# Kernel optimization log

Hardware: AMD Instinct MI355X
Metric: run time of the kernel (lower is better)

Reference implementation:

```python
import jax, jax.numpy as jnp
import numpy as np

EPS = 1e-6
LN3 = 1.0986122886681098  # ternary_softmax uses base-3 exponentials: 3**x / sum(3**x)
ROPE_BASE = 10000.0


def exact_rmsnorm(x, g):
    # ExactRMSNorm: x / sqrt(mean(x^2) + eps) * g
    ms = jnp.mean(jnp.square(x), axis=-1, keepdims=True)
    return x * jax.lax.rsqrt(ms + EPS) * g


def ternary_rope(t):
    # Rotary embedding whose cos/sin tables are quantized to {-1, 0, +1}
    # (round() of cos/sin in [-1,1] yields exactly the ternary set).
    S, D = t.shape[-2], t.shape[-1]
    half = D // 2
    inv_freq = 1.0 / (ROPE_BASE ** (jnp.arange(half, dtype=jnp.float32) / half))
    ang = jnp.arange(S, dtype=jnp.float32)[:, None] * inv_freq[None, :]  # [S, half]
    cos = jnp.round(jnp.cos(ang))
    sin = jnp.round(jnp.sin(ang))
    cos = jnp.concatenate([cos, cos], axis=-1)  # [S, D]
    sin = jnp.concatenate([sin, sin], axis=-1)
    rot = jnp.concatenate([-t[..., half:], t[..., :half]], axis=-1)
    return t * cos + rot * sin


def ternary_softmax(x, axis=-1):
    # softmax in base 3: 3**x / sum(3**x) == softmax(x * ln 3)
    return jax.nn.softmax(x * LN3, axis=axis)


def setup_inputs() -> dict:
    key = jax.random.key(0)
    ks = jax.random.split(key, 6)
    B, S, D = 4, 4096, 1024
    x = jax.random.normal(ks[0], (B, S, D), dtype=jnp.float32)
    g_norm = jnp.ones((D,), dtype=jnp.float32)
    w_qkv = jax.random.normal(ks[1], (D, 3 * D), dtype=jnp.float32) * 0.02
    b_qkv = jnp.zeros((3 * D,), dtype=jnp.float32)
    w_proj = jax.random.normal(ks[2], (D, D), dtype=jnp.float32) * 0.02
    b_proj = jnp.zeros((D,), dtype=jnp.float32)
    return {"x": x, "g_norm": g_norm, "w_qkv": w_qkv, "b_qkv": b_qkv,
            "w_proj": w_proj, "b_proj": b_proj}


def reference(x, g_norm, w_qkv, b_qkv, w_proj, b_proj):
    D = x.shape[-1]
    scale = 1.0 / jnp.sqrt(jnp.float32(D))
    residual = x
    h = exact_rmsnorm(x, g_norm)
    qkv = h @ w_qkv + b_qkv  # [B, S, 3D]
    q, k, v = jnp.split(qkv, 3, axis=-1)
    q = ternary_rope(q)
    k = ternary_rope(k)
    scores = jnp.einsum("bsd,btd->bst", q, k) * scale  # [B, S, S]
    attn = ternary_softmax(scores, axis=-1)
    o = jnp.einsum("bst,btd->bsd", attn, v)
    return o @ w_proj + b_proj + residual
```

## Files before the change

kernel.cpp:

```cpp
#include <hip/hip_runtime.h>
#include <hip/hip_fp8.h>
#include <stdint.h>

#define DEVI __device__ __forceinline__

typedef unsigned short u16;
typedef uint8_t u8;
typedef __attribute__((ext_vector_type(8))) __bf16 bf16x8;
typedef __attribute__((ext_vector_type(4))) float f32x4;
typedef __attribute__((ext_vector_type(4))) int i32x4;
typedef __attribute__((ext_vector_type(8))) int i32x8;

DEVI float b2f(u16 u) { union { unsigned int i; float f; } v; v.i = ((unsigned int)u) << 16; return v.f; }
DEVI u16 f2b(float f) {
  union { float f; unsigned int i; } v; v.f = f;
  unsigned int r = v.i + 0x7fffu + ((v.i >> 16) & 1u);
  return (u16)(r >> 16);
}
DEVI u8 f2f8(float f) { __hip_fp8_e4m3 t(f); return t.__x; }

DEVI void gld_lds16(const void* g, void* l) {
  __builtin_amdgcn_global_load_lds((const __attribute__((address_space(1))) unsigned int*)g,
                                   (__attribute__((address_space(3))) unsigned int*)l, 16, 0, 0);
}

DEVI i32x8 ld32(const u8* p0, const u8* p1) {
  i32x4 lo = *(const i32x4*)p0;
  i32x4 hi = *(const i32x4*)p1;
  return __builtin_shufflevector(lo, hi, 0, 1, 2, 3, 4, 5, 6, 7);
}


__global__ __launch_bounds__(256) void k_rmsnorm(const float* __restrict__ x,
                                                 const float* __restrict__ g,
                                                 u8* __restrict__ h) {
  const int row = blockIdx.x;
  const int t = threadIdx.x;
  const float4 v = ((const float4*)(x + (size_t)row * 1024))[t];
  float ss = v.x * v.x + v.y * v.y + v.z * v.z + v.w * v.w;
  for (int off = 32; off > 0; off >>= 1) ss += __shfl_down(ss, off);
  __shared__ float red[4];
  if ((t & 63) == 0) red[t >> 6] = ss;
  __syncthreads();
  const float tot = red[0] + red[1] + red[2] + red[3];
  const float sc = rsqrtf(tot * (1.0f / 1024.0f) + 1e-6f);
  const float4 gv = ((const float4*)g)[t];
  uchar4 o;
  o.x = f2f8(v.x * sc * gv.x); o.y = f2f8(v.y * sc * gv.y);
  o.z = f2f8(v.z * sc * gv.z); o.w = f2f8(v.w * sc * gv.w);
  *(uchar4*)(h + (size_t)row * 1024 + t * 4) = o;
}

__global__ __launch_bounds__(256) void k_transpose_cast(const float* __restrict__ src,
                                                        int rows, int cols,
                                                        u16* __restrict__ dst) {
  __shared__ float tile[32][33];
  const int c0 = blockIdx.x * 32, r0 = blockIdx.y * 32;
  const int tx = threadIdx.x, ty = threadIdx.y;
  for (int i = 0; i < 32; i += 8)
    tile[ty + i][tx] = src[(size_t)(r0 + ty + i) * cols + c0 + tx];
  __syncthreads();
  for (int i = 0; i < 32; i += 8)
    dst[(size_t)(c0 + ty + i) * rows + r0 + tx] = f2b(tile[tx][ty + i]);
}

__global__ __launch_bounds__(256) void k_transpose_cast_f8(const float* __restrict__ src,
                                                           int rows, int cols,
                                                           u8* __restrict__ dst) {
  __shared__ float tile[32][33];
  const int c0 = blockIdx.x * 32, r0 = blockIdx.y * 32;
  const int tx = threadIdx.x, ty = threadIdx.y;
  for (int i = 0; i < 32; i += 8)
    tile[ty + i][tx] = src[(size_t)(r0 + ty + i) * cols + c0 + tx];
  __syncthreads();
  for (int i = 0; i < 32; i += 8)
    dst[(size_t)(c0 + ty + i) * rows + r0 + tx] = f2f8(tile[tx][ty + i] * 32.0f);
}

__global__ __launch_bounds__(256) void k_rope_cast(const u16* __restrict__ q16, const u16* __restrict__ k16,
                                                   u8* __restrict__ q8, u8* __restrict__ k8) {
  const int row = blockIdx.x;
  const int pos = row & 4095;
  const int t = threadIdx.x;
  const int j0 = t * 2;
  float c[2], s[2];
#pragma unroll
  for (int u = 0; u < 2; u++) {
    const float e = (float)(j0 + u) * (1.0f / 512.0f);
    const float invf = exp2f(-13.287712379549449f * e);
    const float ang = (float)pos * invf;
    c[u] = rintf(cosf(ang));
    s[u] = rintf(sinf(ang));
  }
  const u16* qr = q16 + (size_t)row * 1024;
  const u16* kr = k16 + (size_t)row * 1024;
  u8* qo = q8 + (size_t)row * 1024;
  u8* ko = k8 + (size_t)row * 1024;
  const ushort2 qa = *(const ushort2*)(qr + j0), qb = *(const ushort2*)(qr + j0 + 512);
  const ushort2 ka = *(const ushort2*)(kr + j0), kb = *(const ushort2*)(kr + j0 + 512);
  uchar2 o;
  o.x = f2f8(b2f(qa.x) * c[0] - b2f(qb.x) * s[0]);
  o.y = f2f8(b2f(qa.y) * c[1] - b2f(qb.y) * s[1]);
  *(uchar2*)(qo + j0) = o;
  o.x = f2f8(b2f(qb.x) * c[0] + b2f(qa.x) * s[0]);
  o.y = f2f8(b2f(qb.y) * c[1] + b2f(qa.y) * s[1]);
  *(uchar2*)(qo + j0 + 512) = o;
  o.x = f2f8(b2f(ka.x) * c[0] - b2f(kb.x) * s[0]);
  o.y = f2f8(b2f(ka.y) * c[1] - b2f(kb.y) * s[1]);
  *(uchar2*)(ko + j0) = o;
  o.x = f2f8(b2f(kb.x) * c[0] + b2f(ka.x) * s[0]);
  o.y = f2f8(b2f(kb.y) * c[1] + b2f(ka.y) * s[1]);
  *(uchar2*)(ko + j0 + 512) = o;
}

DEVI void gemm_tile(const u16* __restrict__ A, int lda,
                    const u16* __restrict__ B, int ldb,
                    int K, int m0, int n0,
                    u16* As, u16* Bs, f32x4 acc[4][4]) {
  const int t = threadIdx.x;
  const int sr = t >> 2;
  const int sc = (t & 3) * 8;
  const u16* Ag0 = A + (size_t)(m0 + sr) * lda + sc;
  const u16* Ag1 = A + (size_t)(m0 + 64 + sr) * lda + sc;
  const u16* Bg0 = B + (size_t)(n0 + sr) * ldb + sc;
  const u16* Bg1 = B + (size_t)(n0 + 64 + sr) * ldb + sc;
  u16* Asw = As + t * 8;
  u16* Bsw = Bs + t * 8;

  const int lane = t & 63, qd = lane >> 4, l16 = lane & 15;
  const int wave = t >> 6;
  const int wm = (wave >> 1) * 64, wn = (wave & 1) * 64;
  const int aoff = (wm + l16) * 32 + qd * 8;
  const int boff = (wn + l16) * 32 + qd * 8;

  auto stage = [&](int sel, int k0) {
    u16* Ad = Asw + sel * 4096;
    u16* Bd = Bsw + sel * 4096;
    gld_lds16(Ag0 + k0, Ad);
    gld_lds16(Ag1 + k0, Ad + 2048);
    gld_lds16(Bg0 + k0, Bd);
    gld_lds16(Bg1 + k0, Bd + 2048);
  };

  stage(0, 0);
  int cur = 0;
  for (int k0 = 0; k0 < K; k0 += 32) {
    if (k0 + 32 < K) {
      stage(cur ^ 1, k0 + 32);
      asm volatile("s_waitcnt vmcnt(4)" ::: "memory");
    } else {
      asm volatile("s_waitcnt vmcnt(0)" ::: "memory");
    }
    __builtin_amdgcn_s_barrier();
    const u16* Ard = As + cur * 4096 + aoff;
    const u16* Brd = Bs + cur * 4096 + boff;
    bf16x8 af[4], bfv[4];
#pragma unroll
    for (int i = 0; i < 4; i++) af[i] = *(const bf16x8*)(Ard + i * 16 * 32);
#pragma unroll
    for (int j = 0; j < 4; j++) bfv[j] = *(const bf16x8*)(Brd + j * 16 * 32);
    __builtin_amdgcn_s_setprio(1);
#pragma unroll
    for (int i = 0; i < 4; i++)
#pragma unroll
      for (int j = 0; j < 4; j++)
        acc[i][j] = __builtin_amdgcn_mfma_f32_16x16x32_bf16(af[i], bfv[j], acc[i][j], 0, 0, 0);
    __builtin_amdgcn_s_setprio(0);
    __builtin_amdgcn_s_barrier();
    cur ^= 1;
  }
}

DEVI void gemm_tile_mx(const u8* __restrict__ A, int lda,
                       const u8* __restrict__ B, int ldb,
                       int K, int m0, int n0,
                       u8* As, u8* Bs, f32x4 acc[4][4], int sB) {
  const int t = threadIdx.x;
  const int sr = t >> 3;
  const int sc = ((t & 7) ^ (sr & 7)) << 4;
  const u8* Agb = A + (size_t)(m0 + sr) * lda + sc;
  const u8* Bgb = B + (size_t)(n0 + sr) * ldb + sc;
  u8* Asw = As + t * 16;
  u8* Bsw = Bs + t * 16;

  const int lane = t & 63, qd = lane >> 4, l16 = lane & 15;
  const int wave = t >> 6;
  const int wm = (wave >> 1) * 64, wn = (wave & 1) * 64;
  const int key = l16 & 7;
  const int c0 = ((qd << 1) ^ key) << 4;
  const int aoff = (wm + l16) * 128 + c0;
  const int boff = (wn + l16) * 128 + c0;

  auto stage = [&](int sel, int k0) {
    u8* Ad = Asw + sel * 16384;
    u8* Bd = Bsw + sel * 16384;
#pragma unroll
    for (int l = 0; l < 4; l++) {
      gld_lds16(Agb + k0 + (size_t)l * 32 * lda, Ad + l * 4096);
      gld_lds16(Bgb + k0 + (size_t)l * 32 * ldb, Bd + l * 4096);
    }
  };

  stage(0, 0);
  int cur = 0;
  for (int k0 = 0; k0 < K; k0 += 128) {
    if (k0 + 128 < K) {
      stage(cur ^ 1, k0 + 128);
      asm volatile("s_waitcnt vmcnt(8)" ::: "memory");
    } else {
      asm volatile("s_waitcnt vmcnt(0)" ::: "memory");
    }
    __builtin_amdgcn_s_barrier();
    const u8* Ab = As + cur * 16384;
    const u8* Bb = Bs + cur * 16384;
    i32x8 a[4], b[4];
#pragma unroll
    for (int i = 0; i < 4; i++)
      a[i] = ld32(Ab + aoff + i * 2048, Ab + (aoff ^ 16) + i * 2048);
#pragma unroll
    for (int j = 0; j < 4; j++)
      b[j] = ld32(Bb + boff + j * 2048, Bb + (boff ^ 16) + j * 2048);
    __builtin_amdgcn_s_setprio(1);
#pragma unroll
    for (int i = 0; i < 4; i++)
#pragma unroll
      for (int j = 0; j < 4; j++)
        acc[i][j] = __builtin_amdgcn_mfma_scale_f32_16x16x128_f8f6f4(
            a[i], b[j], acc[i][j], 0 , 0 ,
            0, 0x7f7f7f7f, 0, sB);
    __builtin_amdgcn_s_setprio(0);
    __builtin_amdgcn_s_barrier();
    cur ^= 1;
  }
}

#define ACC_INIT()                                               \
  f32x4 acc[4][4];                                               \
  _Pragma("unroll") for (int i = 0; i < 4; i++)                  \
      _Pragma("unroll") for (int j = 0; j < 4; j++)              \
          acc[i][j] = f32x4{0.f, 0.f, 0.f, 0.f};

#define GEMM_EPI_IDX()                                           \
  const int t = threadIdx.x, lane = t & 63, qd = lane >> 4,      \
            l16 = lane & 15, wave = t >> 6;                      \
  const int wm = (wave >> 1) * 64, wn = (wave & 1) * 64;         \
  (void)t;


__global__ __launch_bounds__(256) void k_gemm_qkv(const u8* __restrict__ A, const u8* __restrict__ Bt,
                                                  const float* __restrict__ bias,
                                                  u16* __restrict__ q16, u16* __restrict__ k16,
                                                  u8* __restrict__ vt) {
  __shared__ alignas(16) u8 As[32768], Bs[32768];
  ACC_INIT();
  const int bid = blockIdx.y * 24 + blockIdx.x;
  const int xcd = bid & 7, idx = bid >> 3;
  const int m0 = (xcd * 16 + idx / 24) * 128;
  const int n0 = (idx % 24) * 128;
  gemm_tile_mx(A, 1024, Bt, 1024, 1024, m0, n0, As, Bs, acc, 0x7a7a7a7a);
  GEMM_EPI_IDX();
  const int sec = n0 >> 10;
  const int nb0 = n0 & 1023;
  if (sec < 2) {
    u16* dst = (sec == 0) ? q16 : k16;
#pragma unroll
    for (int i = 0; i < 4; i++) {
      const int mb = m0 + wm + i * 16 + qd * 4;
#pragma unroll
      for (int j = 0; j < 4; j++) {
        const int col = n0 + wn + j * 16 + l16;
        const float bv = bias[col];
        const int dcol = nb0 + wn + j * 16 + l16;
#pragma unroll
        for (int r = 0; r < 4; r++)
          dst[(size_t)(mb + r) * 1024 + dcol] = f2b(acc[i][j][r] + bv);
      }
    }
  } else {
    u8* T = As;
    const int STR = 144;
#pragma unroll
    for (int i = 0; i < 4; i++) {
      const int mloc = wm + i * 16 + qd * 4;
#pragma unroll
      for (int j = 0; j < 4; j++) {
        const int dloc = wn + j * 16 + l16;
        const float bv = bias[n0 + wn + j * 16 + l16];
#pragma unroll
        for (int r = 0; r < 4; r++)
          T[dloc * STR + mloc + r] = f2f8(acc[i][j][r] + bv);
      }
    }
    __syncthreads();
    const int b = m0 >> 12;
    const int s0 = m0 & 4095;
    const int row = t >> 1, half = (t & 1) * 64;
    u8* dst = vt + ((size_t)(b * 1024 + nb0 + row)) * 4096 + s0 + half;
#pragma unroll
    for (int c = 0; c < 4; c++)
      *(i32x4*)(dst + c * 16) = *(const i32x4*)(T + row * STR + half + c * 16);
  }
}

__global__ __launch_bounds__(256) void k_gemm_scores(const u8* __restrict__ q, const u8* __restrict__ kk,
                                                     u8* __restrict__ P, float* __restrict__ ls) {
  __shared__ alignas(16) u8 As[32768], Bs[32768];
  ACC_INIT();
  const int b = blockIdx.z;
  const u8* A = q + (size_t)b * 4096 * 1024;
  const u8* Bt = kk + (size_t)b * 4096 * 1024;
  const int bid = blockIdx.y * 32 + blockIdx.x;
  const int xcd = bid & 7, idx = bid >> 3;
  const int m0 = ((xcd >> 2) * 16 + (idx & 15)) * 128;
  const int n0 = ((xcd & 3) * 8 + (idx >> 4)) * 128;
  gemm_tile_mx(A, 1024, Bt, 1024, 1024, m0, n0, As, Bs, acc, 0x7f7f7f7f);
  GEMM_EPI_IDX();
  const float C3 = 0.04953007814753613f;
  const size_t Pb = (size_t)b * 4096 * 4096;
  f32x4 rowp[4];
#pragma unroll
  for (int i = 0; i < 4; i++) rowp[i] = f32x4{0.f, 0.f, 0.f, 0.f};
#pragma unroll
  for (int i = 0; i < 4; i++) {
    const int mb = m0 + wm + i * 16 + qd * 4;
#pragma unroll
    for (int j = 0; j < 4; j++) {
      const int col = n0 + wn + j * 16 + l16;
#pragma unroll
      for (int r = 0; r < 4; r++) {
        const float pv = __builtin_amdgcn_exp2f(acc[i][j][r] * C3);
        P[Pb + (size_t)(mb + r) * 4096 + col] = f2f8(pv);
        rowp[i][r] += pv;
      }
    }
  }
#pragma unroll
  for (int m = 1; m < 16; m <<= 1)
#pragma unroll
    for (int i = 0; i < 4; i++) {
      rowp[i].x += __shfl_xor(rowp[i].x, m);
      rowp[i].y += __shfl_xor(rowp[i].y, m);
      rowp[i].z += __shfl_xor(rowp[i].z, m);
      rowp[i].w += __shfl_xor(rowp[i].w, m);
    }
  if (l16 == 0) {
#pragma unroll
    for (int i = 0; i < 4; i++) {
      const int mb = m0 + wm + i * 16 + qd * 4;
#pragma unroll
      for (int r = 0; r < 4; r++)
        atomicAdd(ls + (size_t)b * 4096 + mb + r, rowp[i][r]);
    }
  }
}

__global__ __launch_bounds__(256) void k_gemm_pv(const u8* __restrict__ P, const u8* __restrict__ vt,
                                                 const float* __restrict__ ls, u16* __restrict__ o) {
  __shared__ alignas(16) u8 As[32768], Bs[32768];
  ACC_INIT();
  const int b = blockIdx.z;
  const u8* A = P + (size_t)b * 4096 * 4096;
  const u8* Bt = vt + (size_t)b * 1024 * 4096;
  const int bid = blockIdx.y * 8 + blockIdx.x;
  const int xcd = bid & 7, idx = bid >> 3;
  const int m0 = ((xcd >> 1) * 8 + (idx & 7)) * 128;
  const int n0 = ((xcd & 1) * 4 + (idx >> 3)) * 128;
  gemm_tile_mx(A, 4096, Bt, 4096, 4096, m0, n0, As, Bs, acc, 0x7f7f7f7f);
  GEMM_EPI_IDX();
#pragma unroll
  for (int i = 0; i < 4; i++) {
    const int mb = m0 + wm + i * 16 + qd * 4;
    f32x4 inv;
#pragma unroll
    for (int r = 0; r < 4; r++) inv[r] = 1.0f / ls[(size_t)b * 4096 + mb + r];
#pragma unroll
    for (int j = 0; j < 4; j++) {
      const int col = n0 + wn + j * 16 + l16;
#pragma unroll
      for (int r = 0; r < 4; r++)
        o[(size_t)(b * 4096 + mb + r) * 1024 + col] = f2b(acc[i][j][r] * inv[r]);
    }
  }
}

__global__ __launch_bounds__(256) void k_gemm_proj(const u16* __restrict__ A, const u16* __restrict__ Bt,
                                                   const float* __restrict__ bias, const float* __restrict__ x,
                                                   float* __restrict__ out) {
  __shared__ alignas(16) u16 As[8192], Bs[8192];
  ACC_INIT();
  const int bid = blockIdx.y * 8 + blockIdx.x;
  const int xcd = bid & 7, idx = bid >> 3;
  const int m0 = (xcd * 16 + idx / 8) * 128;
  const int n0 = (idx % 8) * 128;
  gemm_tile(A, 1024, Bt, 1024, 1024, m0, n0, As, Bs, acc);
  GEMM_EPI_IDX();
#pragma unroll
  for (int i = 0; i < 4; i++) {
    const int mb = m0 + wm + i * 16 + qd * 4;
#pragma unroll
    for (int j = 0; j < 4; j++) {
      const int col = n0 + wn + j * 16 + l16;
      const float bv = bias[col];
#pragma unroll
      for (int r = 0; r < 4; r++) {
        const size_t idxo = (size_t)(mb + r) * 1024 + col;
        out[idxo] = acc[i][j][r] + bv + x[idxo];
      }
    }
  }
}

extern "C" void kernel_launch(void* const* d_in, const int* in_sizes, int n_in,
                              void* d_out, int out_size, void* d_ws, size_t ws_size,
                              hipStream_t stream) {
  const float* x     = (const float*)d_in[0];
  const float* g     = (const float*)d_in[1];
  const float* wqkv  = (const float*)d_in[2];
  const float* bqkv  = (const float*)d_in[3];
  const float* wproj = (const float*)d_in[4];
  const float* bproj = (const float*)d_in[5];
  float* out = (float*)d_out;

  char* wsp = (char*)d_ws;
  size_t off = 0;
  auto take = [&](size_t bytes) -> void* {
    off = (off + 255) & ~(size_t)255;
    void* r = wsp + off;
    off += bytes;
    return r;
  };
  char* hreg = (char*)take(16384ull * 1024 * 2);
  u8*  h8   = (u8*)hreg;
  u16* o16  = (u16*)hreg;
  u8*  wqT8 = (u8*)take(3072ull * 1024);
  u16* wpT  = (u16*)take(1024ull * 1024 * 2);
  u8*  q8   = (u8*)take(16384ull * 1024);
  u8*  k8   = (u8*)take(16384ull * 1024);
  u8*  vt   = (u8*)take(4ull * 1024 * 4096);
  float* ls = (float*)take(16384ull * 4);
  char* scratch = (char*)take(3ull * 16384 * 1024 * 2);
  u16* q16 = (u16*)scratch;
  u16* k16 = (u16*)(scratch + 16384ull * 1024 * 2);
  u8*  P   = (u8*)scratch;

  k_transpose_cast_f8<<<dim3(3072 / 32, 1024 / 32), dim3(32, 8), 0, stream>>>(wqkv, 1024, 3072, wqT8);
  k_transpose_cast<<<dim3(1024 / 32, 1024 / 32), dim3(32, 8), 0, stream>>>(wproj, 1024, 1024, wpT);
  k_rmsnorm<<<16384, 256, 0, stream>>>(x, g, h8);
  k_gemm_qkv<<<dim3(24, 128), 256, 0, stream>>>(h8, wqT8, bqkv, q16, k16, vt);
  k_rope_cast<<<16384, 256, 0, stream>>>(q16, k16, q8, k8);
  hipMemsetAsync(ls, 0, 16384 * 4, stream);
  k_gemm_scores<<<dim3(32, 32, 4), 256, 0, stream>>>(q8, k8, P, ls);
  k_gemm_pv<<<dim3(8, 32, 4), 256, 0, stream>>>(P, vt, ls, o16);
  k_gemm_proj<<<dim3(8, 128), 256, 0, stream>>>(o16, wpT, bproj, x, out);
}
```

Before: 450.6 us.

## Fuse ternary RoPE into QKV GEMM epilogue via permuted weight columns

Permutes the Q/K columns of the transposed fp8 QKV weight so each rotary pair lands in adjacent lanes. The GEMM epilogue then applies the rotation with a lane shuffle and a precomputed ternary cos/sin table, writing fp8 Q/K directly. This removes the separate rope_cast kernel and the bf16 Q/K round trip through global memory. In exchange it adds a small table-building kernel and per-element table loads and byte-sized scattered stores in the epilogue.

Result: no change. 455.6 us (+1.1%).

```diff
diff --git a/kernel.cpp b/kernel.cpp
--- a/kernel.cpp
+++ b/kernel.cpp
@@ -64,6 +64,13 @@
     dst[(size_t)(c0 + ty + i) * rows + r0 + tx] = f2b(tile[tx][ty + i]);
 }
 
+DEVI int rope_perm(int c) {
+  if (c >= 2048) return c;
+  const int sec = c >> 10, cc = c & 1023;
+  const int slot = (cc < 512) ? (cc << 1) : (((cc - 512) << 1) | 1);
+  return (sec << 10) | slot;
+}
+
 __global__ __launch_bounds__(256) void k_transpose_cast_f8(const float* __restrict__ src,
                                                            int rows, int cols,
                                                            u8* __restrict__ dst) {
@@ -74,43 +81,23 @@
     tile[ty + i][tx] = src[(size_t)(r0 + ty + i) * cols + c0 + tx];
   __syncthreads();
   for (int i = 0; i < 32; i += 8)
-    dst[(size_t)(c0 + ty + i) * rows + r0 + tx] = f2f8(tile[tx][ty + i] * 32.0f);
-}
-
-__global__ __launch_bounds__(256) void k_rope_cast(const u16* __restrict__ q16, const u16* __restrict__ k16,
-                                                   u8* __restrict__ q8, u8* __restrict__ k8) {
-  const int row = blockIdx.x;
-  const int pos = row & 4095;
+    dst[(size_t)rope_perm(c0 + ty + i) * rows + r0 + tx] = f2f8(tile[tx][ty + i] * 32.0f);
+}
+
+__global__ __launch_bounds__(256) void k_rope_table(char2* __restrict__ tab) {
+  const int pos = blockIdx.x;
   const int t = threadIdx.x;
-  const int j0 = t * 2;
-  float c[2], s[2];
 #pragma unroll
   for (int u = 0; u < 2; u++) {
-    const float e = (float)(j0 + u) * (1.0f / 512.0f);
+    const int m = t * 2 + u;
+    const float e = (float)m * (1.0f / 512.0f);
     const float invf = exp2f(-13.287712379549449f * e);
     const float ang = (float)pos * invf;
-    c[u] = rintf(cosf(ang));
-    s[u] = rintf(sinf(ang));
-  }
-  const u16* qr = q16 + (size_t)row * 1024;
-  const u16* kr = k16 + (size_t)row * 1024;
-  u8* qo = q8 + (size_t)row * 1024;
-  u8* ko = k8 + (size_t)row * 1024;
-  const ushort2 qa = *(const ushort2*)(qr + j0), qb = *(const ushort2*)(qr + j0 + 512);
-  const ushort2 ka = *(const ushort2*)(kr + j0), kb = *(const ushort2*)(kr + j0 + 512);
-  uchar2 o;
-  o.x = f2f8(b2f(qa.x) * c[0] - b2f(qb.x) * s[0]);
-  o.y = f2f8(b2f(qa.y) * c[1] - b2f(qb.y) * s[1]);
-  *(uchar2*)(qo + j0) = o;
-  o.x = f2f8(b2f(qb.x) * c[0] + b2f(qa.x) * s[0]);
-  o.y = f2f8(b2f(qb.y) * c[1] + b2f(qa.y) * s[1]);
-  *(uchar2*)(qo + j0 + 512) = o;
-  o.x = f2f8(b2f(ka.x) * c[0] - b2f(kb.x) * s[0]);
-  o.y = f2f8(b2f(ka.y) * c[1] - b2f(kb.y) * s[1]);
-  *(uchar2*)(ko + j0) = o;
-  o.x = f2f8(b2f(kb.x) * c[0] + b2f(ka.x) * s[0]);
-  o.y = f2f8(b2f(kb.y) * c[1] + b2f(ka.y) * s[1]);
-  *(uchar2*)(ko + j0 + 512) = o;
+    char2 cs;
+    cs.x = (char)rintf(cosf(ang));
+    cs.y = (char)rintf(sinf(ang));
+    tab[(size_t)pos * 512 + m] = cs;
+  }
 }
 
 DEVI void gemm_tile(const u16* __restrict__ A, int lda,
@@ -249,7 +236,8 @@
 
 __global__ __launch_bounds__(256) void k_gemm_qkv(const u8* __restrict__ A, const u8* __restrict__ Bt,
                                                   const float* __restrict__ bias,
-                                                  u16* __restrict__ q16, u16* __restrict__ k16,
+                                                  const char2* __restrict__ tab,
+                                                  u8* __restrict__ q8, u8* __restrict__ k8,
                                                   u8* __restrict__ vt) {
   __shared__ alignas(16) u8 As[32768], Bs[32768];
   ACC_INIT();
@@ -262,18 +250,28 @@
   const int sec = n0 >> 10;
   const int nb0 = n0 & 1023;
   if (sec < 2) {
-    u16* dst = (sec == 0) ? q16 : k16;
+    u8* dst = (sec == 0) ? q8 : k8;
 #pragma unroll
     for (int i = 0; i < 4; i++) {
       const int mb = m0 + wm + i * 16 + qd * 4;
 #pragma unroll
       for (int j = 0; j < 4; j++) {
-        const int col = n0 + wn + j * 16 + l16;
-        const float bv = bias[col];
-        const int dcol = nb0 + wn + j * 16 + l16;
-#pragma unroll
-        for (int r = 0; r < 4; r++)
-          dst[(size_t)(mb + r) * 1024 + dcol] = f2b(acc[i][j][r] + bv);
+        const int pc = nb0 + wn + j * 16 + l16;
+        const int m = pc >> 1;
+        const int par = pc & 1;
+        const int ocol = m + (par << 9);
+        const float bv = bias[(sec << 10) + ocol];
+#pragma unroll
+        for (int r = 0; r < 4; r++) {
+          const int row = mb + r;
+          const int pos = row & 4095;
+          const float v = acc[i][j][r] + bv;
+          const float p = __shfl_xor(v, 1);
+          const char2 cs = tab[(size_t)pos * 512 + m];
+          const float c = (float)cs.x, s = (float)cs.y;
+          const float out = par ? (v * c + p * s) : (v * c - p * s);
+          dst[(size_t)row * 1024 + ocol] = f2f8(out);
+        }
       }
     }
   } else {
@@ -295,10 +293,10 @@
     const int b = m0 >> 12;
     const int s0 = m0 & 4095;
     const int row = t >> 1, half = (t & 1) * 64;
-    u8* dst = vt + ((size_t)(b * 1024 + nb0 + row)) * 4096 + s0 + half;
+    u8* dstv = vt + ((size_t)(b * 1024 + (n0 & 1023) + row)) * 4096 + s0 + half;
 #pragma unroll
     for (int c = 0; c < 4; c++)
-      *(i32x4*)(dst + c * 16) = *(const i32x4*)(T + row * STR + half + c * 16);
+      *(i32x4*)(dstv + c * 16) = *(const i32x4*)(T + row * STR + half + c * 16);
   }
 }
 
@@ -438,16 +436,14 @@
   u8*  k8   = (u8*)take(16384ull * 1024);
   u8*  vt   = (u8*)take(4ull * 1024 * 4096);
   float* ls = (float*)take(16384ull * 4);
-  char* scratch = (char*)take(3ull * 16384 * 1024 * 2);
-  u16* q16 = (u16*)scratch;
-  u16* k16 = (u16*)(scratch + 16384ull * 1024 * 2);
-  u8*  P   = (u8*)scratch;
-
+  char2* tab = (char2*)take(4096ull * 512 * 2);
+  u8* P = (u8*)take(4ull * 4096 * 4096);
+
+  k_rope_table<<<4096, 256, 0, stream>>>(tab);
   k_transpose_cast_f8<<<dim3(3072 / 32, 1024 / 32), dim3(32, 8), 0, stream>>>(wqkv, 1024, 3072, wqT8);
   k_transpose_cast<<<dim3(1024 / 32, 1024 / 32), dim3(32, 8), 0, stream>>>(wproj, 1024, 1024, wpT);
   k_rmsnorm<<<16384, 256, 0, stream>>>(x, g, h8);
-  k_gemm_qkv<<<dim3(24, 128), 256, 0, stream>>>(h8, wqT8, bqkv, q16, k16, vt);
-  k_rope_cast<<<16384, 256, 0, stream>>>(q16, k16, q8, k8);
+  k_gemm_qkv<<<dim3(24, 128), 256, 0, stream>>>(h8, wqT8, bqkv, tab, q8, k8, vt);
   hipMemsetAsync(ls, 0, 16384 * 4, stream);
   k_gemm_scores<<<dim3(32, 32, 4), 256, 0, stream>>>(q8, k8, P, ls);
   k_gemm_pv<<<dim3(8, 32, 4), 256, 0, stream>>>(P, vt, ls, o16);
```
